# Optimization experiments

Measured on AMD Instinct MI355X. Metric: run time of the kernel, lower is better.

The kernel has to match this reference:

```python
import jax, jax.numpy as jnp
import numpy as np

B, N, DIM, INTER, HEAD = 2, 2048, 1024, 1024, 16
N_SEG = 4


def setup_inputs() -> dict:
    key = jax.random.key(0)
    k0, k1, k2, k3 = jax.random.split(key, 4)
    features = jax.random.normal(k0, (B, N, DIM), dtype=jnp.float32)
    mask = jax.random.randint(k1, (B, N, N), 0, N_SEG, dtype=jnp.int32)
    W_qkv = jax.random.normal(k2, (DIM, 3 * INTER), dtype=jnp.float32) * 0.02
    W_out = jax.random.normal(k3, (INTER, DIM), dtype=jnp.float32) * 0.02
    return {"features": features, "mask": mask, "W_qkv": W_qkv, "W_out": W_out,
            "n_segments": N_SEG}


def reference(features, mask, W_qkv, W_out, n_segments):
    b, n, dim = features.shape
    h = HEAD
    scale = INTER ** (-0.5)  # NOTE: original scales by inter_dim, not per-head dim
    qkv = features @ W_qkv                              # [b, n, 3*inter]
    q, k, v = jnp.split(qkv, 3, axis=-1)
    q = q.reshape(b, n, h, -1)                          # [b, n, h, d]
    k = k.reshape(b, n, h, -1)
    v = v.reshape(b, n, h, -1)
    alpha = jnp.einsum('bihd,bjhd->bhij', q, k) * scale  # [b, h, n, n]
    exps = jnp.exp(alpha)
    out = jnp.zeros((b, n, h, v.shape[-1]), dtype=features.dtype)
    # loop over fixed small segment-id set; ids absent from mask contribute 0,
    # exactly matching the torch.unique loop in the original.
    for seg in range(n_segments):
        m = (mask == seg)[:, None, :, :]                # [b, 1, n, n] -> broadcast over h
        fe = jnp.where(m, exps, 0.0)
        s = jnp.sum(fe, axis=-1, keepdims=True)
        att = fe / jnp.where(s == 0, 1.0, s)            # masked softmax (no max-shift, faithful)
        out = out + jnp.einsum('bhij,bjhd->bihd', att, v)
    out = out.reshape(b, n, h * v.shape[-1])            # [b, n, inter]
    return out @ W_out                                  # dropout at eval = identity
```

## Files before the change

kernel.cpp:

```cpp
#include <hip/hip_runtime.h>
#include <hip/hip_bf16.h>

#define BB 2
#define NN 2048
#define DIM 1024
#define INTER 1024
#define NHEAD 16
#define HDIM 64
#define NSEG 4
#define QKVW (3 * INTER)

typedef __attribute__((ext_vector_type(8))) short bf16x8;
typedef __attribute__((ext_vector_type(4))) float f32x4;

static __device__ __forceinline__ unsigned short f2bf(float f) {
    __hip_bfloat16 h = __float2bfloat16(f);
    return *reinterpret_cast<unsigned short*>(&h);
}
static __device__ __forceinline__ float bf2f(unsigned short u) {
    unsigned int x = ((unsigned int)u) << 16;
    return __builtin_bit_cast(float, x);
}
static __device__ __forceinline__ unsigned int pack_bf16_rn(float lo, float hi) {
    unsigned int u = __builtin_bit_cast(unsigned int, lo) + 0x8000u;
    unsigned int v = __builtin_bit_cast(unsigned int, hi) + 0x8000u;
    return __builtin_amdgcn_perm(v, u, 0x07060302u);
}

__global__ __launch_bounds__(256) void prep_fused(
        const float* __restrict__ features, unsigned short* __restrict__ featb,
        const int* __restrict__ mask, unsigned char* __restrict__ maskb,
        const float* __restrict__ W_qkv, unsigned short* __restrict__ wqt,
        const float* __restrict__ W_out, unsigned short* __restrict__ woh,
        unsigned short* __restrict__ wol) {
    __shared__ float tile[64][65];
    const int bid = blockIdx.x;
    const int t = threadIdx.x;

    if (bid < 4096) {
        int i = (bid * 256 + t) * 4;
        float4 v = *(const float4*)&features[i];
        ushort4 o = {f2bf(v.x), f2bf(v.y), f2bf(v.z), f2bf(v.w)};
        *(ushort4*)&featb[i] = o;
        return;
    }
    if (bid < 6144) {
        size_t i = (size_t)((bid - 4096) * 256 + t) * 16;
        int4 a = *(const int4*)&mask[i];
        int4 b = *(const int4*)&mask[i + 4];
        int4 c = *(const int4*)&mask[i + 8];
        int4 d = *(const int4*)&mask[i + 12];
        uint4 p;
        p.x = (unsigned)(a.x & 3) | ((unsigned)(a.y & 3) << 8) | ((unsigned)(a.z & 3) << 16) | ((unsigned)(a.w & 3) << 24);
        p.y = (unsigned)(b.x & 3) | ((unsigned)(b.y & 3) << 8) | ((unsigned)(b.z & 3) << 16) | ((unsigned)(b.w & 3) << 24);
        p.z = (unsigned)(c.x & 3) | ((unsigned)(c.y & 3) << 8) | ((unsigned)(c.z & 3) << 16) | ((unsigned)(c.w & 3) << 24);
        p.w = (unsigned)(d.x & 3) | ((unsigned)(d.y & 3) << 8) | ((unsigned)(d.z & 3) << 16) | ((unsigned)(d.w & 3) << 24);
        *(uint4*)&maskb[i] = p;
        return;
    }
    if (bid < 6912) {
        const int id = bid - 6144;
        const int c0 = (id % 48) * 64, r0 = (id / 48) * 64;
        const int R = DIM, C = QKVW;
#pragma unroll
        for (int it = 0; it < 4; ++it) {
            int r = it * 16 + (t >> 4);
            int c = (t & 15) * 4;
            float4 v = *(const float4*)&W_qkv[(size_t)(r0 + r) * C + c0 + c];
            tile[r][c] = v.x; tile[r][c + 1] = v.y; tile[r][c + 2] = v.z; tile[r][c + 3] = v.w;
        }
        __syncthreads();
#pragma unroll
        for (int it = 0; it < 4; ++it) {
            int c = it * 16 + (t >> 4);
            int r = (t & 15) * 4;
            ushort4 o = {f2bf(tile[r][c]), f2bf(tile[r + 1][c]), f2bf(tile[r + 2][c]), f2bf(tile[r + 3][c])};
            *(ushort4*)&wqt[(size_t)(c0 + c) * R + r0 + r] = o;
        }
        return;
    }
    {
        const int id = bid - 6912;
        const int c0 = (id % 16) * 64, r0 = (id / 16) * 64;
        const int R = INTER, C = DIM;
#pragma unroll
        for (int it = 0; it < 4; ++it) {
            int r = it * 16 + (t >> 4);
            int c = (t & 15) * 4;
            float4 v = *(const float4*)&W_out[(size_t)(r0 + r) * C + c0 + c];
            tile[r][c] = v.x; tile[r][c + 1] = v.y; tile[r][c + 2] = v.z; tile[r][c + 3] = v.w;
        }
        __syncthreads();
#pragma unroll
        for (int it = 0; it < 4; ++it) {
            int c = it * 16 + (t >> 4);
            int r = (t & 15) * 4;
            float v0 = tile[r][c], v1 = tile[r + 1][c], v2 = tile[r + 2][c], v3 = tile[r + 3][c];
            ushort4 hh, ll;
            hh.x = f2bf(v0); ll.x = f2bf(v0 - bf2f(hh.x));
            hh.y = f2bf(v1); ll.y = f2bf(v1 - bf2f(hh.y));
            hh.z = f2bf(v2); ll.z = f2bf(v2 - bf2f(hh.z));
            hh.w = f2bf(v3); ll.w = f2bf(v3 - bf2f(hh.w));
            *(ushort4*)&woh[(size_t)(c0 + c) * R + r0 + r] = hh;
            *(ushort4*)&wol[(size_t)(c0 + c) * R + r0 + r] = ll;
        }
    }
}

#define GBK 32

__global__ __launch_bounds__(256) void gemm_qkv_mfma(
        const unsigned short* __restrict__ A,
        const unsigned short* __restrict__ Bt,
        unsigned short* __restrict__ Cqk,
        unsigned short* __restrict__ Vtg) {
    const int K = 1024;
    __shared__ __align__(16) unsigned short As[128][GBK];
    __shared__ __align__(16) unsigned short Bs[128][GBK];
    const int t = threadIdx.x;
    const int w = t >> 6, lane = t & 63, l15 = lane & 15, quad = lane >> 4;
    const int wr = w >> 1, wc = w & 1;
    const int row0 = blockIdx.y * 128, col0 = blockIdx.x * 128;
    const int lrow = lane >> 2;
    const int lkof = (lane & 3) * 8;

    f32x4 acc[4][4];
#pragma unroll
    for (int i = 0; i < 4; ++i)
#pragma unroll
        for (int j = 0; j < 4; ++j) acc[i][j] = (f32x4){0.f, 0.f, 0.f, 0.f};

    for (int k0 = 0; k0 < K; k0 += GBK) {
#pragma unroll
        for (int c = 0; c < 2; ++c) {
            int rbase = w * 32 + c * 16;
            const unsigned short* ga = A  + (size_t)(row0 + rbase + lrow) * K + k0 + lkof;
            const unsigned short* gb = Bt + (size_t)(col0 + rbase + lrow) * K + k0 + lkof;
            __builtin_amdgcn_global_load_lds(
                (const __attribute__((address_space(1))) void*)ga,
                (__attribute__((address_space(3))) void*)&As[rbase][0], 16, 0, 0);
            __builtin_amdgcn_global_load_lds(
                (const __attribute__((address_space(1))) void*)gb,
                (__attribute__((address_space(3))) void*)&Bs[rbase][0], 16, 0, 0);
        }
        __syncthreads();
        bf16x8 af[4], bfr[4];
#pragma unroll
        for (int i = 0; i < 4; ++i) af[i]  = *(const bf16x8*)&As[wr * 64 + i * 16 + l15][quad * 8];
#pragma unroll
        for (int j = 0; j < 4; ++j) bfr[j] = *(const bf16x8*)&Bs[wc * 64 + j * 16 + l15][quad * 8];
#pragma unroll
        for (int i = 0; i < 4; ++i)
#pragma unroll
            for (int j = 0; j < 4; ++j)
                acc[i][j] = __builtin_amdgcn_mfma_f32_16x16x32_bf16(af[i], bfr[j], acc[i][j], 0, 0, 0);
        __syncthreads();
    }

    if (col0 < 2048) {
        const float qs = (col0 < 1024) ? 0.04508422f : 1.0f;
#pragma unroll
        for (int i = 0; i < 4; ++i)
#pragma unroll
            for (int j = 0; j < 4; ++j)
#pragma unroll
                for (int r = 0; r < 4; ++r) {
                    int row = row0 + wr * 64 + i * 16 + quad * 4 + r;
                    int col = col0 + wc * 64 + j * 16 + l15;
                    Cqk[(size_t)row * 2048 + col] = f2bf(acc[i][j][r] * qs);
                }
    } else {
#pragma unroll
        for (int i = 0; i < 4; ++i)
#pragma unroll
            for (int j = 0; j < 4; ++j) {
                int col = col0 + wc * 64 + j * 16 + l15 - 2048;
                int row = row0 + wr * 64 + i * 16 + quad * 4;
                int bb = row >> 11, n = row & 2047;
                ushort4 o = {f2bf(acc[i][j][0]), f2bf(acc[i][j][1]),
                             f2bf(acc[i][j][2]), f2bf(acc[i][j][3])};
                *(ushort4*)&Vtg[((size_t)bb * INTER + col) * NN + n] = o;
            }
    }
}

__global__ __launch_bounds__(256) void gemm_out2(
        const unsigned short* __restrict__ Ah,
        const unsigned short* __restrict__ Bh,
        const unsigned short* __restrict__ Bl,
        float* __restrict__ C) {
    const int K = INTER, N = DIM;
    __shared__ __align__(16) unsigned short Ash[128][32];
    __shared__ __align__(16) unsigned short Bsh[64][32];
    __shared__ __align__(16) unsigned short Bsl[64][32];
    const int t = threadIdx.x;
    const int w = t >> 6, lane = t & 63, l15 = lane & 15, quad = lane >> 4;
    const int wr = w >> 1, wc = w & 1;
    const int row0 = blockIdx.y * 128, col0 = blockIdx.x * 64;
    const int lrow = lane >> 2, lkof = (lane & 3) * 8;

    f32x4 acc[4][2];
#pragma unroll
    for (int i = 0; i < 4; ++i)
#pragma unroll
        for (int j = 0; j < 2; ++j) acc[i][j] = (f32x4){0.f, 0.f, 0.f, 0.f};

    for (int k0 = 0; k0 < K; k0 += 32) {
#pragma unroll
        for (int c = 0; c < 2; ++c) {
            int rbase = w * 32 + c * 16;
            const unsigned short* gah = Ah + (size_t)(row0 + rbase + lrow) * K + k0 + lkof;
            __builtin_amdgcn_global_load_lds(
                (const __attribute__((address_space(1))) void*)gah,
                (__attribute__((address_space(3))) void*)&Ash[rbase][0], 16, 0, 0);
        }
        {
            int rbase = w * 16;
            const unsigned short* gbh = Bh + (size_t)(col0 + rbase + lrow) * K + k0 + lkof;
            const unsigned short* gbl = Bl + (size_t)(col0 + rbase + lrow) * K + k0 + lkof;
            __builtin_amdgcn_global_load_lds(
                (const __attribute__((address_space(1))) void*)gbh,
                (__attribute__((address_space(3))) void*)&Bsh[rbase][0], 16, 0, 0);
            __builtin_amdgcn_global_load_lds(
                (const __attribute__((address_space(1))) void*)gbl,
                (__attribute__((address_space(3))) void*)&Bsl[rbase][0], 16, 0, 0);
        }
        __syncthreads();
        bf16x8 ah[4], bh[2], bl[2];
#pragma unroll
        for (int i = 0; i < 4; ++i)
            ah[i] = *(const bf16x8*)&Ash[wr * 64 + i * 16 + l15][quad * 8];
#pragma unroll
        for (int j = 0; j < 2; ++j) {
            bh[j] = *(const bf16x8*)&Bsh[wc * 32 + j * 16 + l15][quad * 8];
            bl[j] = *(const bf16x8*)&Bsl[wc * 32 + j * 16 + l15][quad * 8];
        }
#pragma unroll
        for (int i = 0; i < 4; ++i)
#pragma unroll
            for (int j = 0; j < 2; ++j) {
                acc[i][j] = __builtin_amdgcn_mfma_f32_16x16x32_bf16(ah[i], bh[j], acc[i][j], 0, 0, 0);
                acc[i][j] = __builtin_amdgcn_mfma_f32_16x16x32_bf16(ah[i], bl[j], acc[i][j], 0, 0, 0);
            }
        __syncthreads();
    }
#pragma unroll
    for (int i = 0; i < 4; ++i)
#pragma unroll
        for (int j = 0; j < 2; ++j)
#pragma unroll
            for (int r = 0; r < 4; ++r)
                C[(size_t)(row0 + wr * 64 + i * 16 + quad * 4 + r) * N +
                  col0 + wc * 32 + j * 16 + l15] = acc[i][j][r];
}

__global__ __launch_bounds__(256, 3) void attn_seg_mfma(
        const unsigned short* __restrict__ qk,
        const unsigned short* __restrict__ vtg,
        const unsigned char* __restrict__ maskb,
        unsigned short* __restrict__ ctxh) {
    __shared__ __align__(16) unsigned short KsL[2 * 4096];
    __shared__ __align__(16) unsigned short VtL[2 * 4096];
    __shared__ __align__(16) unsigned char  MbL[2 * 5120];
    __shared__ __align__(16) unsigned short El4[4 * 1024];

    const int t    = threadIdx.x;
    const int w    = t >> 6;
    const int lane = t & 63;
    const int l15  = lane & 15;
    const int quad = lane >> 4;
    const int ksw  = (l15 & 7) << 3;
    const int i0   = blockIdx.x * 64;
    const int hh   = blockIdx.y;
    const int b    = blockIdx.z;

    const int c0   = (quad * 8) ^ ksw;
    const int c1   = (32 + quad * 8) ^ ksw;
    const int a0   = l15 * 64 + c0;
    const int a1   = l15 * 64 + c1;
    const int wEl  = w * 1024;
    int ew[4];
#pragma unroll
    for (int nt = 0; nt < 4; ++nt) ew[nt] = l15 * 64 + ((nt * 16 + quad * 4) ^ ksw);
    const int ef0 = wEl + l15 * 64 + c0;
    const int ef1 = wEl + l15 * 64 + c1;
    const int mrd = (w * 16 + l15) * 80 + quad * 8;

    const int skey = t >> 3, sdc = (t & 7) * 8;
    const int ssw  = sdc ^ ((skey & 7) << 3);
    const int sdst = t * 8;
    const unsigned short* pK0 = qk + (size_t)(b * NN + skey) * 2048 + 1024 + hh * HDIM + ssw;
    const unsigned short* pK1 = pK0 + (size_t)32 * 2048;
    const unsigned short* pV0 = vtg + ((size_t)b * INTER + hh * HDIM + skey) * NN + ssw;
    const unsigned short* pV1 = pV0 + (size_t)32 * NN;
    const unsigned char* pM = maskb + (size_t)(b * NN + i0 + (t >> 2)) * NN + (t & 3) * 16;
    const int wM = (t >> 2) * 80 + (t & 3) * 16;

    bf16x8 qa0, qa1;
    {
        const unsigned short* qp =
            qk + (size_t)(b * NN + i0 + w * 16 + l15) * 2048 + hh * HDIM + quad * 8;
        qa0 = *(const bf16x8*)qp;
        qa1 = *(const bf16x8*)(qp + 32);
    }

    bf16x8 onesb;
    {
        short ob = (l15 == 0) ? (short)0x3F80 : (short)0;
#pragma unroll
        for (int j = 0; j < 8; ++j) onesb[j] = ob;
    }

    f32x4 acc[NSEG][5];
#pragma unroll
    for (int m = 0; m < NSEG; ++m)
#pragma unroll
        for (int nt = 0; nt < 5; ++nt) acc[m][nt] = (f32x4){0.f, 0.f, 0.f, 0.f};

    auto stage = [&](int bb) {
        const int kb = (bb << 12) + sdst;
        __builtin_amdgcn_global_load_lds(
            (const __attribute__((address_space(1))) void*)pK0,
            (__attribute__((address_space(3))) void*)&KsL[kb], 16, 0, 0);
        __builtin_amdgcn_global_load_lds(
            (const __attribute__((address_space(1))) void*)pK1,
            (__attribute__((address_space(3))) void*)&KsL[kb + 2048], 16, 0, 0);
        __builtin_amdgcn_global_load_lds(
            (const __attribute__((address_space(1))) void*)pV0,
            (__attribute__((address_space(3))) void*)&VtL[kb], 16, 0, 0);
        __builtin_amdgcn_global_load_lds(
            (const __attribute__((address_space(1))) void*)pV1,
            (__attribute__((address_space(3))) void*)&VtL[kb + 2048], 16, 0, 0);
        *(uint4*)&MbL[bb * 5120 + wM] = *(const uint4*)pM;
        pK0 += (size_t)64 * 2048; pK1 += (size_t)64 * 2048;
        pV0 += 64; pV1 += 64;
        pM += 64;
    };

    stage(0);

    for (int jt = 0; jt < NN / 64; ++jt) {
        __syncthreads();
        if (jt + 1 < NN / 64) stage((jt + 1) & 1);
        const int bbase = (jt & 1) << 12;
        const int mbase = (jt & 1) * 5120;

#pragma unroll
        for (int nt = 0; nt < 4; ++nt) {
            f32x4 s = {0.f, 0.f, 0.f, 0.f};
            bf16x8 kb0 = *(const bf16x8*)&KsL[bbase + a0 + nt * 1024];
            bf16x8 kb1 = *(const bf16x8*)&KsL[bbase + a1 + nt * 1024];
            s = __builtin_amdgcn_mfma_f32_16x16x32_bf16(kb0, qa0, s, 0, 0, 0);
            s = __builtin_amdgcn_mfma_f32_16x16x32_bf16(kb1, qa1, s, 0, 0, 0);
            float e0 = __builtin_amdgcn_exp2f(s[0]);
            float e1 = __builtin_amdgcn_exp2f(s[1]);
            float e2 = __builtin_amdgcn_exp2f(s[2]);
            float e3 = __builtin_amdgcn_exp2f(s[3]);
            uint2 pk;
            pk.x = pack_bf16_rn(e0, e1);
            pk.y = pack_bf16_rn(e2, e3);
            *(uint2*)&El4[wEl + ew[nt]] = pk;
        }

#pragma unroll
        for (int ks = 0; ks < 2; ++ks) {
            union { int4 i; bf16x8 v; } ef;
            ef.i = *(const int4*)&El4[ks ? ef1 : ef0];
            uint2 sbv = *(const uint2*)&MbL[mbase + mrd + ks * 32];
            unsigned int dup[4];
            dup[0] = __builtin_amdgcn_perm(0u, sbv.x, 0x01010000u);
            dup[1] = __builtin_amdgcn_perm(0u, sbv.x, 0x03030202u);
            dup[2] = __builtin_amdgcn_perm(0u, sbv.y, 0x01010000u);
            dup[3] = __builtin_amdgcn_perm(0u, sbv.y, 0x03030202u);
            const unsigned int* ed = (const unsigned int*)&ef.i;
            bf16x8 vb[4];
#pragma unroll
            for (int nt = 0; nt < 4; ++nt)
                vb[nt] = *(const bf16x8*)&VtL[bbase + (ks ? a1 : a0) + nt * 1024];
            __builtin_amdgcn_s_setprio(1);
#pragma unroll
            for (int m = 0; m < NSEG; ++m) {
                const unsigned int Tm = 0xFFu << (8 * m);
                union { int4 i; bf16x8 v; } wm;
#pragma unroll
                for (int d = 0; d < 4; ++d)
                    ((unsigned int*)&wm.i)[d] = ed[d] & __builtin_amdgcn_perm(0u, Tm, dup[d]);
#pragma unroll
                for (int nt = 0; nt < 4; ++nt)
                    acc[m][nt] = __builtin_amdgcn_mfma_f32_16x16x32_bf16(wm.v, vb[nt], acc[m][nt], 0, 0, 0);
                acc[m][4] = __builtin_amdgcn_mfma_f32_16x16x32_bf16(wm.v, onesb, acc[m][4], 0, 0, 0);
            }
            __builtin_amdgcn_s_setprio(0);
        }
    }

    float rres[NSEG][4];
#pragma unroll
    for (int m = 0; m < NSEG; ++m)
#pragma unroll
        for (int r = 0; r < 4; ++r) {
            float sum = __shfl(acc[m][4][r], lane & 48, 64);
            rres[m][r] = (sum > 0.f) ? (1.f / sum) : 0.f;
        }
#pragma unroll
    for (int nt = 0; nt < 4; ++nt)
#pragma unroll
        for (int r = 0; r < 4; ++r) {
            float v = acc[0][nt][r] * rres[0][r] + acc[1][nt][r] * rres[1][r] +
                      acc[2][nt][r] * rres[2][r] + acc[3][nt][r] * rres[3][r];
            size_t idx = (size_t)(b * NN + i0 + w * 16 + quad * 4 + r) * INTER +
                         hh * HDIM + nt * 16 + l15;
            ctxh[idx] = f2bf(v);
        }
}

extern "C" void kernel_launch(void* const* d_in, const int* in_sizes, int n_in,
                              void* d_out, int out_size, void* d_ws, size_t ws_size,
                              hipStream_t stream) {
    const float* features = (const float*)d_in[0];
    const int*   mask     = (const int*)d_in[1];
    const float* W_qkv    = (const float*)d_in[2];
    const float* W_out    = (const float*)d_in[3];
    float* out = (float*)d_out;

    const int M = BB * NN;
    char* ws = (char*)d_ws;
    unsigned short* qk2  = (unsigned short*)ws;
    ws += (size_t)M * 2048 * 2;
    unsigned short* vtg  = (unsigned short*)ws;
    ws += (size_t)BB * INTER * NN * 2;
    unsigned short* ctxh = (unsigned short*)ws;
    ws += (size_t)M * INTER * 2;
    unsigned short* featb = (unsigned short*)ws;
    ws += (size_t)M * DIM * 2;
    unsigned short* wqt = (unsigned short*)ws;
    ws += (size_t)QKVW * DIM * 2;
    unsigned char* maskb = (unsigned char*)ws;
    ws += (size_t)BB * NN * NN;
    unsigned short* woh = (unsigned short*)ws;
    ws += (size_t)DIM * INTER * 2;
    unsigned short* wol = (unsigned short*)ws;
    ws += (size_t)DIM * INTER * 2;

    dim3 blk(256);

    prep_fused<<<dim3(7168), blk, 0, stream>>>(
        features, featb, mask, maskb, W_qkv, wqt, W_out, woh, wol);

    gemm_qkv_mfma<<<dim3(QKVW / 128, M / 128), blk, 0, stream>>>(featb, wqt, qk2, vtg);

    attn_seg_mfma<<<dim3(NN / 64, NHEAD, BB), blk, 0, stream>>>(qk2, vtg, maskb, ctxh);

    gemm_out2<<<dim3(DIM / 64, M / 128), blk, 0, stream>>>(
        ctxh, woh, wol, out);
}
```

Before: 259.5 us.

## Drop bf16 lo-split of W_out and derive last segment from unmasked totals

The output GEMM no longer uses the hi/lo bf16 split of W_out. It does a single bf16 MFMA pass, halving that GEMM's B-operand traffic and MFMA count, and prep no longer writes the low-part weights. In attention, segment 3 is no longer masked separately. Its accumulators use the unmasked exp tile, and its contribution comes from subtraction (total minus segments 0-2), with the reciprocal weights adjusted to match. This saves mask-building work per k-step, but the subtraction and the lower W_out precision both add rounding error.

Measured after the change: 253.4 us. 1.02x faster.

```diff
diff --git a/kernel.cpp b/kernel.cpp
--- a/kernel.cpp
+++ b/kernel.cpp
@@ -31,8 +31,7 @@
         const float* __restrict__ features, unsigned short* __restrict__ featb,
         const int* __restrict__ mask, unsigned char* __restrict__ maskb,
         const float* __restrict__ W_qkv, unsigned short* __restrict__ wqt,
-        const float* __restrict__ W_out, unsigned short* __restrict__ woh,
-        unsigned short* __restrict__ wol) {
+        const float* __restrict__ W_out, unsigned short* __restrict__ woh) {
     __shared__ float tile[64][65];
     const int bid = blockIdx.x;
     const int t = threadIdx.x;
@@ -58,52 +57,32 @@
         *(uint4*)&maskb[i] = p;
         return;
     }
+    const float* src;
+    unsigned short* dst;
+    int R, C, c0, r0;
     if (bid < 6912) {
         const int id = bid - 6144;
-        const int c0 = (id % 48) * 64, r0 = (id / 48) * 64;
-        const int R = DIM, C = QKVW;
-#pragma unroll
-        for (int it = 0; it < 4; ++it) {
-            int r = it * 16 + (t >> 4);
-            int c = (t & 15) * 4;
-            float4 v = *(const float4*)&W_qkv[(size_t)(r0 + r) * C + c0 + c];
-            tile[r][c] = v.x; tile[r][c + 1] = v.y; tile[r][c + 2] = v.z; tile[r][c + 3] = v.w;
-        }
-        __syncthreads();
-#pragma unroll
-        for (int it = 0; it < 4; ++it) {
-            int c = it * 16 + (t >> 4);
-            int r = (t & 15) * 4;
-            ushort4 o = {f2bf(tile[r][c]), f2bf(tile[r + 1][c]), f2bf(tile[r + 2][c]), f2bf(tile[r + 3][c])};
-            *(ushort4*)&wqt[(size_t)(c0 + c) * R + r0 + r] = o;
-        }
-        return;
-    }
-    {
+        src = W_qkv; dst = wqt; R = DIM; C = QKVW;
+        c0 = (id % 48) * 64; r0 = (id / 48) * 64;
+    } else {
         const int id = bid - 6912;
-        const int c0 = (id % 16) * 64, r0 = (id / 16) * 64;
-        const int R = INTER, C = DIM;
-#pragma unroll
-        for (int it = 0; it < 4; ++it) {
-            int r = it * 16 + (t >> 4);
-            int c = (t & 15) * 4;
-            float4 v = *(const float4*)&W_out[(size_t)(r0 + r) * C + c0 + c];
-            tile[r][c] = v.x; tile[r][c + 1] = v.y; tile[r][c + 2] = v.z; tile[r][c + 3] = v.w;
-        }
-        __syncthreads();
-#pragma unroll
-        for (int it = 0; it < 4; ++it) {
-            int c = it * 16 + (t >> 4);
-            int r = (t & 15) * 4;
-            float v0 = tile[r][c], v1 = tile[r + 1][c], v2 = tile[r + 2][c], v3 = tile[r + 3][c];
-            ushort4 hh, ll;
-            hh.x = f2bf(v0); ll.x = f2bf(v0 - bf2f(hh.x));
-            hh.y = f2bf(v1); ll.y = f2bf(v1 - bf2f(hh.y));
-            hh.z = f2bf(v2); ll.z = f2bf(v2 - bf2f(hh.z));
-            hh.w = f2bf(v3); ll.w = f2bf(v3 - bf2f(hh.w));
-            *(ushort4*)&woh[(size_t)(c0 + c) * R + r0 + r] = hh;
-            *(ushort4*)&wol[(size_t)(c0 + c) * R + r0 + r] = ll;
-        }
+        src = W_out; dst = woh; R = INTER; C = DIM;
+        c0 = (id % 16) * 64; r0 = (id / 16) * 64;
+    }
+#pragma unroll
+    for (int it = 0; it < 4; ++it) {
+        int r = it * 16 + (t >> 4);
+        int c = (t & 15) * 4;
+        float4 v = *(const float4*)&src[(size_t)(r0 + r) * C + c0 + c];
+        tile[r][c] = v.x; tile[r][c + 1] = v.y; tile[r][c + 2] = v.z; tile[r][c + 3] = v.w;
+    }
+    __syncthreads();
+#pragma unroll
+    for (int it = 0; it < 4; ++it) {
+        int c = it * 16 + (t >> 4);
+        int r = (t & 15) * 4;
+        ushort4 o = {f2bf(tile[r][c]), f2bf(tile[r + 1][c]), f2bf(tile[r + 2][c]), f2bf(tile[r + 3][c])};
+        *(ushort4*)&dst[(size_t)(c0 + c) * R + r0 + r] = o;
     }
 }
 
@@ -184,15 +163,13 @@
     }
 }
 
-__global__ __launch_bounds__(256) void gemm_out2(
+__global__ __launch_bounds__(256) void gemm_out1(
         const unsigned short* __restrict__ Ah,
         const unsigned short* __restrict__ Bh,
-        const unsigned short* __restrict__ Bl,
         float* __restrict__ C) {
     const int K = INTER, N = DIM;
     __shared__ __align__(16) unsigned short Ash[128][32];
     __shared__ __align__(16) unsigned short Bsh[64][32];
-    __shared__ __align__(16) unsigned short Bsl[64][32];
     const int t = threadIdx.x;
     const int w = t >> 6, lane = t & 63, l15 = lane & 15, quad = lane >> 4;
     const int wr = w >> 1, wc = w & 1;
@@ -217,31 +194,23 @@
         {
             int rbase = w * 16;
             const unsigned short* gbh = Bh + (size_t)(col0 + rbase + lrow) * K + k0 + lkof;
-            const unsigned short* gbl = Bl + (size_t)(col0 + rbase + lrow) * K + k0 + lkof;
             __builtin_amdgcn_global_load_lds(
                 (const __attribute__((address_space(1))) void*)gbh,
                 (__attribute__((address_space(3))) void*)&Bsh[rbase][0], 16, 0, 0);
-            __builtin_amdgcn_global_load_lds(
-                (const __attribute__((address_space(1))) void*)gbl,
-                (__attribute__((address_space(3))) void*)&Bsl[rbase][0], 16, 0, 0);
         }
         __syncthreads();
-        bf16x8 ah[4], bh[2], bl[2];
+        bf16x8 ah[4], bh[2];
 #pragma unroll
         for (int i = 0; i < 4; ++i)
             ah[i] = *(const bf16x8*)&Ash[wr * 64 + i * 16 + l15][quad * 8];
 #pragma unroll
-        for (int j = 0; j < 2; ++j) {
+        for (int j = 0; j < 2; ++j)
             bh[j] = *(const bf16x8*)&Bsh[wc * 32 + j * 16 + l15][quad * 8];
-            bl[j] = *(const bf16x8*)&Bsl[wc * 32 + j * 16 + l15][quad * 8];
-        }
 #pragma unroll
         for (int i = 0; i < 4; ++i)
 #pragma unroll
-            for (int j = 0; j < 2; ++j) {
+            for (int j = 0; j < 2; ++j)
                 acc[i][j] = __builtin_amdgcn_mfma_f32_16x16x32_bf16(ah[i], bh[j], acc[i][j], 0, 0, 0);
-                acc[i][j] = __builtin_amdgcn_mfma_f32_16x16x32_bf16(ah[i], bl[j], acc[i][j], 0, 0, 0);
-            }
         __syncthreads();
     }
 #pragma unroll
@@ -379,7 +348,7 @@
                 vb[nt] = *(const bf16x8*)&VtL[bbase + (ks ? a1 : a0) + nt * 1024];
             __builtin_amdgcn_s_setprio(1);
 #pragma unroll
-            for (int m = 0; m < NSEG; ++m) {
+            for (int m = 0; m < 3; ++m) {
                 const unsigned int Tm = 0xFFu << (8 * m);
                 union { int4 i; bf16x8 v; } wm;
 #pragma unroll
@@ -390,18 +359,28 @@
                     acc[m][nt] = __builtin_amdgcn_mfma_f32_16x16x32_bf16(wm.v, vb[nt], acc[m][nt], 0, 0, 0);
                 acc[m][4] = __builtin_amdgcn_mfma_f32_16x16x32_bf16(wm.v, onesb, acc[m][4], 0, 0, 0);
             }
+#pragma unroll
+            for (int nt = 0; nt < 4; ++nt)
+                acc[3][nt] = __builtin_amdgcn_mfma_f32_16x16x32_bf16(ef.v, vb[nt], acc[3][nt], 0, 0, 0);
+            acc[3][4] = __builtin_amdgcn_mfma_f32_16x16x32_bf16(ef.v, onesb, acc[3][4], 0, 0, 0);
             __builtin_amdgcn_s_setprio(0);
         }
     }
 
     float rres[NSEG][4];
 #pragma unroll
-    for (int m = 0; m < NSEG; ++m)
-#pragma unroll
-        for (int r = 0; r < 4; ++r) {
-            float sum = __shfl(acc[m][4][r], lane & 48, 64);
-            rres[m][r] = (sum > 0.f) ? (1.f / sum) : 0.f;
-        }
+    for (int r = 0; r < 4; ++r) {
+        float d0 = __shfl(acc[0][4][r], lane & 48, 64);
+        float d1 = __shfl(acc[1][4][r], lane & 48, 64);
+        float d2 = __shfl(acc[2][4][r], lane & 48, 64);
+        float dF = __shfl(acc[3][4][r], lane & 48, 64);
+        float d3 = dF - d0 - d1 - d2;
+        float r3 = (d3 > 0.f) ? (1.f / d3) : 0.f;
+        rres[3][r] = r3;
+        rres[0][r] = ((d0 > 0.f) ? (1.f / d0) : 0.f) - r3;
+        rres[1][r] = ((d1 > 0.f) ? (1.f / d1) : 0.f) - r3;
+        rres[2][r] = ((d2 > 0.f) ? (1.f / d2) : 0.f) - r3;
+    }
 #pragma unroll
     for (int nt = 0; nt < 4; ++nt)
 #pragma unroll
@@ -439,18 +418,16 @@
     ws += (size_t)BB * NN * NN;
     unsigned short* woh = (unsigned short*)ws;
     ws += (size_t)DIM * INTER * 2;
-    unsigned short* wol = (unsigned short*)ws;
-    ws += (size_t)DIM * INTER * 2;
 
     dim3 blk(256);
 
     prep_fused<<<dim3(7168), blk, 0, stream>>>(
-        features, featb, mask, maskb, W_qkv, wqt, W_out, woh, wol);
+        features, featb, mask, maskb, W_qkv, wqt, W_out, woh);
 
     gemm_qkv_mfma<<<dim3(QKVW / 128, M / 128), blk, 0, stream>>>(featb, wqt, qk2, vtg);
 
     attn_seg_mfma<<<dim3(NN / 64, NHEAD, BB), blk, 0, stream>>>(qk2, vtg, maskb, ctxh);
 
-    gemm_out2<<<dim3(DIM / 64, M / 128), blk, 0, stream>>>(
-        ctxh, woh, wol, out);
-}
+    gemm_out1<<<dim3(DIM / 64, M / 128), blk, 0, stream>>>(
+        ctxh, woh, out);
+}
```
